# Kernel optimization log

Hardware: AMD Instinct MI355X
Metric: run time of the kernel (lower is better)

The kernel has to match this reference:

```python
import jax, jax.numpy as jnp
import numpy as np


def setup_inputs() -> dict:
    key = jax.random.key(0)
    ks = jax.random.split(key, 7)
    C = 256
    Cqk = C // 8  # 32
    B, D, H, W = 4, 16, 16, 16
    s_in = 1.0 / np.sqrt(C)  # conv1x1 fan_in = C
    return {
        "x": jax.random.normal(ks[0], (B, C, D, H, W), dtype=jnp.float32),
        "Wq": jax.random.uniform(ks[1], (Cqk, C), jnp.float32, -s_in, s_in),
        "bq": jax.random.uniform(ks[2], (Cqk,), jnp.float32, -s_in, s_in),
        "Wk": jax.random.uniform(ks[3], (Cqk, C), jnp.float32, -s_in, s_in),
        "bk": jax.random.uniform(ks[4], (Cqk,), jnp.float32, -s_in, s_in),
        "Wv": jax.random.uniform(ks[5], (C, C), jnp.float32, -s_in, s_in),
        "bv": jax.random.uniform(ks[6], (C,), jnp.float32, -s_in, s_in),
    }


def reference(x, Wq, bq, Wk, bk, Wv, bv):
    B, C, D, H, W = x.shape
    N = D * H * W
    xf = x.reshape(B, C, N)  # [B, C, N]
    # 1x1x1 convs == per-voxel GEMMs over the channel dim
    q = jnp.einsum('oc,bcn->bon', Wq, xf) + bq[None, :, None]  # [B, Cqk, N]
    k = jnp.einsum('oc,bcn->bon', Wk, xf) + bk[None, :, None]  # [B, Cqk, N]
    v = jnp.einsum('oc,bcn->bon', Wv, xf) + bv[None, :, None]  # [B, C, N]
    # attention[b, n, m] = softmax_m( q[:, n] . k[:, m] )
    scores = jnp.einsum('bcn,bcm->bnm', q, k)  # [B, N, N]
    attn = jax.nn.softmax(scores, axis=-1)
    # out = value @ attention^T  -> out[b, c, n] = sum_m v[b,c,m] * attn[b,n,m]
    out = jnp.einsum('bcm,bnm->bcn', v, attn)
    return x + out.reshape(B, C, D, H, W)
```

## Files before the change

kernel.cpp:

```cpp
#include <hip/hip_runtime.h>
#include <math.h>

#define B_   4
#define C_   256
#define CQK  32
#define N_   4096
#define TQ   64
#define TM   64
#define ITERS (N_ / TM)
#define PSS  72

typedef __attribute__((ext_vector_type(8))) short short8;
typedef __attribute__((ext_vector_type(4))) short short4v;
typedef __attribute__((ext_vector_type(4))) float f32x4;
typedef __attribute__((ext_vector_type(2))) unsigned int uint2v;

#if __has_builtin(__builtin_amdgcn_exp2f)
#define EXP2F(x) __builtin_amdgcn_exp2f(x)
#else
#define EXP2F(x) exp2f(x)
#endif

__device__ __forceinline__ unsigned short f2bf(float f) {
    unsigned u = __builtin_bit_cast(unsigned, f);
    u += 0x7fffu + ((u >> 16) & 1u);
    return (unsigned short)(u >> 16);
}

__device__ __forceinline__ unsigned pack2bf(float a, float b) {
    unsigned ua = __builtin_bit_cast(unsigned, a) + 0x8000u;
    unsigned ub = __builtin_bit_cast(unsigned, b) + 0x8000u;
#if __has_builtin(__builtin_amdgcn_perm)
    return __builtin_amdgcn_perm(ub, ua, 0x07060302u);
#else
    return (ua >> 16) | (ub & 0xffff0000u);
#endif
}

__global__ __launch_bounds__(256) void cvt_w(
    const float* __restrict__ Wq, const float* __restrict__ bq,
    const float* __restrict__ Wk, const float* __restrict__ bk,
    const float* __restrict__ Wv, const float* __restrict__ bv,
    unsigned short* __restrict__ wbf, float* __restrict__ biasf)
{
    const float LOG2E = 1.4426950408889634f;
    const int r = blockIdx.x;
    const int t = threadIdx.x;
    const float* src = (r < 32) ? (Wq + r * C_)
                     : (r < 64) ? (Wk + (r - 32) * C_)
                                : (Wv + (r - 64) * C_);
    const float scale = (r < 32) ? LOG2E : 1.0f;
    wbf[r * C_ + t] = f2bf(src[t] * scale);
    if (t == 0)
        biasf[r] = (r < 32) ? bq[r] * LOG2E : (r < 64) ? bk[r - 32] : bv[r - 64];
}

__global__ __launch_bounds__(256, 2) void proj_qkv(
    const float* __restrict__ x, const unsigned short* __restrict__ wbf,
    const float* __restrict__ biasf,
    unsigned short* __restrict__ qb, unsigned short* __restrict__ kb,
    unsigned short* __restrict__ vb)
{
    __shared__ __align__(16) unsigned short qks[32 * 72];

    const int t    = threadIdx.x;
    const int w    = t >> 6;
    const int lane = t & 63;
    const int quad = lane >> 4;
    const int c16  = lane & 15;
    const int n0   = blockIdx.x * 32;
    const int b    = blockIdx.y;

    f32x4 acc[5][2];
#pragma unroll
    for (int i = 0; i < 5; ++i)
#pragma unroll
        for (int nt = 0; nt < 2; ++nt) acc[i][nt] = (f32x4){0.f, 0.f, 0.f, 0.f};

    const float* xb = x + (size_t)(b * C_) * N_ + n0 + c16;
    const unsigned short* wr = wbf + (size_t)(80 * w + c16) * C_ + quad * 8;

#pragma unroll
    for (int h = 0; h < 2; ++h) {
        short8 af[5][4];
#pragma unroll
        for (int i = 0; i < 5; ++i)
#pragma unroll
            for (int k4 = 0; k4 < 4; ++k4)
                af[i][k4] = *(const short8*)(wr + (size_t)(16 * i) * C_ + 128 * h + 32 * k4);
#pragma unroll
        for (int k4 = 0; k4 < 4; ++k4) {
            short8 bf[2];
#pragma unroll
            for (int nt = 0; nt < 2; ++nt) {
                const float* xc = xb + (size_t)(128 * h + 32 * k4 + 8 * quad) * N_ + 16 * nt;
#pragma unroll
                for (int j = 0; j < 8; ++j)
                    bf[nt][j] = (short)f2bf(xc[(size_t)j * N_]);
            }
#pragma unroll
            for (int i = 0; i < 5; ++i)
#pragma unroll
                for (int nt = 0; nt < 2; ++nt)
                    acc[i][nt] = __builtin_amdgcn_mfma_f32_16x16x32_bf16(af[i][k4], bf[nt], acc[i][nt], 0, 0, 0);
        }
    }

#pragma unroll
    for (int i = 0; i < 5; ++i) {
        const int OT = 5 * w + i;
        const int obase = OT * 16 + 4 * quad;
        const f32x4 bv4 = *(const f32x4*)&biasf[obase];
#pragma unroll
        for (int nt = 0; nt < 2; ++nt) {
            const int n = n0 + 16 * nt + c16;
            float vals[4];
#pragma unroll
            for (int r = 0; r < 4; ++r) vals[r] = acc[i][nt][r] + bv4[r];
            if (OT >= 4) {
#pragma unroll
                for (int r = 0; r < 4; ++r)
                    vb[((size_t)(b * C_) + obase + r - 64) * N_ + n] = f2bf(vals[r]);
            } else {
                const int row = 16 * nt + c16;
                const int col = (OT < 2 ? 0 : 32) + (OT & 1) * 16 + 4 * quad;
                short4v pk;
#pragma unroll
                for (int r = 0; r < 4; ++r) pk[r] = (short)f2bf(vals[r]);
                *(short4v*)&qks[row * 72 + col] = pk;
            }
        }
    }
    __syncthreads();
    if (w < 2) {
        unsigned short* dst = w ? kb : qb;
        const int coff = w ? 32 : 0;
#pragma unroll
        for (int h = 0; h < 2; ++h) {
            const int n = 16 * h + (lane >> 2);
            const int c = (lane & 3) * 8;
            const short8 v = *(const short8*)&qks[n * 72 + coff + c];
            *(short8*)(dst + ((size_t)(b * N_) + n0 + n) * 32 + c) = v;
        }
    }
}

__global__ __launch_bounds__(256, 1) void attn_kernel(
    const float* __restrict__ x,
    const unsigned short* __restrict__ qg,
    const unsigned short* __restrict__ kg,
    const unsigned short* __restrict__ vg,
    float* __restrict__ out)
{
    __shared__ __align__(16) unsigned short ps[2][TQ * PSS];
    __shared__ float ls[4 * TQ];

    const int t    = threadIdx.x;
    const int w    = t >> 6;
    const int lane = t & 63;
    const int quad = lane >> 4;
    const int c16  = lane & 15;
    const int b    = blockIdx.x & 3;
    const int q0   = (blockIdx.x >> 2) * TQ;
    const int kvc  = w * 16 + 4 * quad;

    const unsigned short* kbase = kg + (size_t)(b * N_) * 32;
    const unsigned short* vbase = vg + (size_t)(b * C_) * N_;

    short8 bq[4];
#pragma unroll
    for (int g = 0; g < 4; ++g)
        bq[g] = *(const short8*)(qg + ((size_t)(b * N_) + q0 + 16 * g + c16) * 32 + quad * 8);

    f32x4 O[4][4];
#pragma unroll
    for (int ct = 0; ct < 4; ++ct)
#pragma unroll
        for (int qt = 0; qt < 4; ++qt) O[ct][qt] = (f32x4){0.f, 0.f, 0.f, 0.f};

    float lacc[4] = {0.f, 0.f, 0.f, 0.f};

    short8 akA, akB, avA[2][4], avB[2][4];
    akA = *(const short8*)(kbase + (size_t)(w * 16 + c16) * 32 + quad * 8);
#pragma unroll
    for (int s = 0; s < 2; ++s)
#pragma unroll
        for (int ct = 0; ct < 4; ++ct)
            avA[s][ct] = *(const short8*)(
                vbase + (size_t)(64 * w + 16 * ct + c16) * N_ + 32 * s + 8 * quad);

    auto chunk = [&](int ic, const short8& akc, const short8 (&avc)[2][4],
                     short8& akn, short8 (&avn)[2][4], int pb) {
        const int icn = (ic + 1 < ITERS) ? ic + 1 : ITERS - 1;
        const size_t kvn = (size_t)icn * TM;
        akn = *(const short8*)(kbase + (kvn + w * 16 + c16) * 32 + quad * 8);
#pragma unroll
        for (int s = 0; s < 2; ++s)
#pragma unroll
            for (int ct = 0; ct < 4; ++ct)
                avn[s][ct] = *(const short8*)(
                    vbase + (size_t)(64 * w + 16 * ct + c16) * N_ + kvn + 32 * s + 8 * quad);

        const f32x4 z = {0.f, 0.f, 0.f, 0.f};
        f32x4 sf[4];
#pragma unroll
        for (int g = 0; g < 4; ++g)
            sf[g] = __builtin_amdgcn_mfma_f32_16x16x32_bf16(akc, bq[g], z, 0, 0, 0);

#pragma unroll
        for (int g = 0; g < 4; ++g) {
            float p[4];
#pragma unroll
            for (int r = 0; r < 4; ++r) p[r] = EXP2F(sf[g][r]);
            lacc[g] += (p[0] + p[1]) + (p[2] + p[3]);
            uint2v u;
            u.x = pack2bf(p[0], p[1]);
            u.y = pack2bf(p[2], p[3]);
            *(uint2v*)&ps[pb][(16 * g + c16) * PSS + kvc] = u;
        }

        __syncthreads();

        short8 bp[4][2];
#pragma unroll
        for (int qt = 0; qt < 4; ++qt)
#pragma unroll
            for (int s = 0; s < 2; ++s)
                bp[qt][s] = *(const short8*)&ps[pb][(16 * qt + c16) * PSS + 32 * s + 8 * quad];
#pragma unroll
        for (int s = 0; s < 2; ++s)
#pragma unroll
            for (int ct = 0; ct < 4; ++ct)
#pragma unroll
                for (int qt = 0; qt < 4; ++qt)
                    O[ct][qt] = __builtin_amdgcn_mfma_f32_16x16x32_bf16(avc[s][ct], bp[qt][s], O[ct][qt], 0, 0, 0);
    };

#pragma unroll 1
    for (int ic = 0; ic < ITERS; ic += 2) {
        chunk(ic,     akA, avA, akB, avB, 0);
        chunk(ic + 1, akB, avB, akA, avA, 1);
    }

#pragma unroll
    for (int g = 0; g < 4; ++g) {
        lacc[g] += __shfl_xor(lacc[g], 16);
        lacc[g] += __shfl_xor(lacc[g], 32);
    }
    if (quad == 0) {
#pragma unroll
        for (int g = 0; g < 4; ++g)
            ls[w * TQ + 16 * g + c16] = lacc[g];
    }
    __syncthreads();

#pragma unroll
    for (int qt = 0; qt < 4; ++qt) {
        const int q = 16 * qt + c16;
        const float li = 1.0f / (ls[q] + ls[TQ + q] + ls[2 * TQ + q] + ls[3 * TQ + q]);
        const int n = q0 + q;
#pragma unroll
        for (int ct = 0; ct < 4; ++ct) {
#pragma unroll
            for (int r = 0; r < 4; ++r) {
                const int c = 64 * w + 16 * ct + 4 * quad + r;
                const size_t idx = ((size_t)(b * C_) + c) * N_ + n;
                out[idx] = x[idx] + O[ct][qt][r] * li;
            }
        }
    }
}

extern "C" void kernel_launch(void* const* d_in, const int* in_sizes, int n_in,
                              void* d_out, int out_size, void* d_ws, size_t ws_size,
                              hipStream_t stream) {
    const float* x  = (const float*)d_in[0];
    const float* Wq = (const float*)d_in[1];
    const float* bq = (const float*)d_in[2];
    const float* Wk = (const float*)d_in[3];
    const float* bk = (const float*)d_in[4];
    const float* Wv = (const float*)d_in[5];
    const float* bv = (const float*)d_in[6];
    float* out = (float*)d_out;

    unsigned short* ws16 = (unsigned short*)d_ws;
    unsigned short* qb  = ws16;
    unsigned short* kb  = qb + (size_t)B_ * N_ * 32;
    unsigned short* vb  = kb + (size_t)B_ * N_ * 32;
    unsigned short* wbf = vb + (size_t)B_ * C_ * N_;
    float* biasf = (float*)(wbf + 320 * C_);

    cvt_w<<<dim3(320), 256, 0, stream>>>(Wq, bq, Wk, bk, Wv, bv, wbf, biasf);
    proj_qkv<<<dim3(N_ / 32, B_), 256, 0, stream>>>(x, wbf, biasf, qb, kb, vb);
    attn_kernel<<<dim3(N_ / TQ * B_), 256, 0, stream>>>(x, qb, kb, vb, out);
}
```

Baseline: 162.0 us.

## Split attention KV range across blocks, stage K/V in LDS, add combine pass

The attention kernel now runs 512-thread blocks over 128 queries with the key range split in two halves across separate blocks. K and V tiles are staged cooperatively in swizzled shared memory with register prefetch instead of per-wave global loads. A new combine kernel merges the two partial outputs and row sums and adds the residual. The projection kernel transposes and converts x into shared memory once and doubles its tile width. The split-KV scheme costs an extra partial-output write and read (one half in bf16) plus another launch, in exchange for better K/V reuse across waves and a different grid shape.

```diff
diff --git a/kernel.cpp b/kernel.cpp
--- a/kernel.cpp
+++ b/kernel.cpp
@@ -5,10 +5,11 @@
 #define C_   256
 #define CQK  32
 #define N_   4096
-#define TQ   64
+#define TQ   128
 #define TM   64
-#define ITERS (N_ / TM)
+#define HITERS ((N_ / 2) / TM)
 #define PSS  72
+#define XTS  264
 
 typedef __attribute__((ext_vector_type(8))) short short8;
 typedef __attribute__((ext_vector_type(4))) short short4v;
@@ -26,7 +27,9 @@
     u += 0x7fffu + ((u >> 16) & 1u);
     return (unsigned short)(u >> 16);
 }
-
+__device__ __forceinline__ float bf2f(unsigned short s) {
+    return __builtin_bit_cast(float, (unsigned)s << 16);
+}
 __device__ __forceinline__ unsigned pack2bf(float a, float b) {
     unsigned ua = __builtin_bit_cast(unsigned, a) + 0x8000u;
     unsigned ub = __builtin_bit_cast(unsigned, b) + 0x8000u;
@@ -61,49 +64,50 @@
     unsigned short* __restrict__ qb, unsigned short* __restrict__ kb,
     unsigned short* __restrict__ vb)
 {
-    __shared__ __align__(16) unsigned short qks[32 * 72];
+    __shared__ __align__(16) unsigned short xT[64 * XTS];
+    __shared__ __align__(16) unsigned short qks[64 * 72];
 
     const int t    = threadIdx.x;
     const int w    = t >> 6;
     const int lane = t & 63;
     const int quad = lane >> 4;
     const int c16  = lane & 15;
-    const int n0   = blockIdx.x * 32;
+    const int n0   = blockIdx.x * 64;
     const int b    = blockIdx.y;
 
-    f32x4 acc[5][2];
+#pragma unroll
+    for (int p = 0; p < 16; ++p) {
+        const int c  = (t >> 2) + 64 * (p >> 2);
+        const int nq = (t & 3) + 4 * (p & 3);
+        const f32x4 xv = *(const f32x4*)&x[((size_t)(b * C_) + c) * N_ + n0 + 4 * nq];
+#pragma unroll
+        for (int j = 0; j < 4; ++j)
+            xT[(4 * nq + j) * XTS + c] = f2bf(xv[j]);
+    }
+    __syncthreads();
+
+    f32x4 acc[5][4];
 #pragma unroll
     for (int i = 0; i < 5; ++i)
 #pragma unroll
-        for (int nt = 0; nt < 2; ++nt) acc[i][nt] = (f32x4){0.f, 0.f, 0.f, 0.f};
-
-    const float* xb = x + (size_t)(b * C_) * N_ + n0 + c16;
+        for (int nt = 0; nt < 4; ++nt) acc[i][nt] = (f32x4){0.f, 0.f, 0.f, 0.f};
+
     const unsigned short* wr = wbf + (size_t)(80 * w + c16) * C_ + quad * 8;
 
 #pragma unroll
-    for (int h = 0; h < 2; ++h) {
-        short8 af[5][4];
+    for (int ks = 0; ks < 8; ++ks) {
+        short8 af[5], bf[4];
 #pragma unroll
         for (int i = 0; i < 5; ++i)
-#pragma unroll
-            for (int k4 = 0; k4 < 4; ++k4)
-                af[i][k4] = *(const short8*)(wr + (size_t)(16 * i) * C_ + 128 * h + 32 * k4);
-#pragma unroll
-        for (int k4 = 0; k4 < 4; ++k4) {
-            short8 bf[2];
-#pragma unroll
-            for (int nt = 0; nt < 2; ++nt) {
-                const float* xc = xb + (size_t)(128 * h + 32 * k4 + 8 * quad) * N_ + 16 * nt;
-#pragma unroll
-                for (int j = 0; j < 8; ++j)
-                    bf[nt][j] = (short)f2bf(xc[(size_t)j * N_]);
-            }
-#pragma unroll
-            for (int i = 0; i < 5; ++i)
-#pragma unroll
-                for (int nt = 0; nt < 2; ++nt)
-                    acc[i][nt] = __builtin_amdgcn_mfma_f32_16x16x32_bf16(af[i][k4], bf[nt], acc[i][nt], 0, 0, 0);
-        }
+            af[i] = *(const short8*)(wr + (size_t)(16 * i) * C_ + 32 * ks);
+#pragma unroll
+        for (int nt = 0; nt < 4; ++nt)
+            bf[nt] = *(const short8*)&xT[(16 * nt + c16) * XTS + ks * 32 + quad * 8];
+#pragma unroll
+        for (int i = 0; i < 5; ++i)
+#pragma unroll
+            for (int nt = 0; nt < 4; ++nt)
+                acc[i][nt] = __builtin_amdgcn_mfma_f32_16x16x32_bf16(af[i], bf[nt], acc[i][nt], 0, 0, 0);
     }
 
 #pragma unroll
@@ -112,7 +116,7 @@
         const int obase = OT * 16 + 4 * quad;
         const f32x4 bv4 = *(const f32x4*)&biasf[obase];
 #pragma unroll
-        for (int nt = 0; nt < 2; ++nt) {
+        for (int nt = 0; nt < 4; ++nt) {
             const int n = n0 + 16 * nt + c16;
             float vals[4];
 #pragma unroll
@@ -136,7 +140,7 @@
         unsigned short* dst = w ? kb : qb;
         const int coff = w ? 32 : 0;
 #pragma unroll
-        for (int h = 0; h < 2; ++h) {
+        for (int h = 0; h < 4; ++h) {
             const int n = 16 * h + (lane >> 2);
             const int c = (lane & 3) * 8;
             const short8 v = *(const short8*)&qks[n * 72 + coff + c];
@@ -145,14 +149,17 @@
     }
 }
 
-__global__ __launch_bounds__(256, 1) void attn_kernel(
-    const float* __restrict__ x,
+__global__ __launch_bounds__(512, 1) void attn_kernel(
     const unsigned short* __restrict__ qg,
     const unsigned short* __restrict__ kg,
     const unsigned short* __restrict__ vg,
-    float* __restrict__ out)
+    float* __restrict__ outp,
+    unsigned short* __restrict__ Op1,
+    float* __restrict__ lp)
 {
-    __shared__ __align__(16) unsigned short ps[2][TQ * PSS];
+    __shared__ __align__(16) unsigned short ks[TM * 40];
+    __shared__ __align__(16) unsigned short vs[C_ * TM];
+    __shared__ __align__(16) unsigned short ps[TQ * PSS];
     __shared__ float ls[4 * TQ];
 
     const int t    = threadIdx.x;
@@ -160,9 +167,15 @@
     const int lane = t & 63;
     const int quad = lane >> 4;
     const int c16  = lane & 15;
-    const int b    = blockIdx.x & 3;
-    const int q0   = (blockIdx.x >> 2) * TQ;
-    const int kvc  = w * 16 + 4 * quad;
+    const int flat = blockIdx.x;
+    const int half = flat & 1;
+    const int b    = (flat >> 1) & 3;
+    const int q0   = (flat >> 3) * TQ;
+    const int kvb0 = half * (N_ / 2);
+    const int f   = w & 3;
+    const int qg_ = w >> 2;
+    const int cs = w & 3;
+    const int pg = w >> 2;
 
     const unsigned short* kbase = kg + (size_t)(b * N_) * 32;
     const unsigned short* vbase = vg + (size_t)(b * C_) * N_;
@@ -170,7 +183,17 @@
     short8 bq[4];
 #pragma unroll
     for (int g = 0; g < 4; ++g)
-        bq[g] = *(const short8*)(qg + ((size_t)(b * N_) + q0 + 16 * g + c16) * 32 + quad * 8);
+        bq[g] = *(const short8*)(qg + ((size_t)(b * N_) + q0 + 16 * (4 * qg_ + g) + c16) * 32 + quad * 8);
+
+    const int vc0 = t >> 3, vj = t & 7;
+    const int kn = t >> 2, kseg = t & 3;
+
+    short8 vpre[4], kpre;
+#pragma unroll
+    for (int p = 0; p < 4; ++p)
+        vpre[p] = *(const short8*)(vbase + (size_t)(vc0 + 64 * p) * N_ + kvb0 + vj * 8);
+    if (t < 256)
+        kpre = *(const short8*)(kbase + (size_t)(kvb0 + kn) * 32 + kseg * 8);
 
     f32x4 O[4][4];
 #pragma unroll
@@ -180,32 +203,23 @@
 
     float lacc[4] = {0.f, 0.f, 0.f, 0.f};
 
-    short8 akA, akB, avA[2][4], avB[2][4];
-    akA = *(const short8*)(kbase + (size_t)(w * 16 + c16) * 32 + quad * 8);
-#pragma unroll
-    for (int s = 0; s < 2; ++s)
-#pragma unroll
-        for (int ct = 0; ct < 4; ++ct)
-            avA[s][ct] = *(const short8*)(
-                vbase + (size_t)(64 * w + 16 * ct + c16) * N_ + 32 * s + 8 * quad);
-
-    auto chunk = [&](int ic, const short8& akc, const short8 (&avc)[2][4],
-                     short8& akn, short8 (&avn)[2][4], int pb) {
-        const int icn = (ic + 1 < ITERS) ? ic + 1 : ITERS - 1;
-        const size_t kvn = (size_t)icn * TM;
-        akn = *(const short8*)(kbase + (kvn + w * 16 + c16) * 32 + quad * 8);
-#pragma unroll
-        for (int s = 0; s < 2; ++s)
-#pragma unroll
-            for (int ct = 0; ct < 4; ++ct)
-                avn[s][ct] = *(const short8*)(
-                    vbase + (size_t)(64 * w + 16 * ct + c16) * N_ + kvn + 32 * s + 8 * quad);
-
+#pragma unroll 1
+    for (int it = 0; it < HITERS; ++it) {
+#pragma unroll
+        for (int p = 0; p < 4; ++p) {
+            const int c = vc0 + 64 * p;
+            *(short8*)&vs[c * TM + 8 * (vj ^ (c & 7))] = vpre[p];
+        }
+        if (t < 256)
+            *(short8*)&ks[kn * 40 + kseg * 8] = kpre;
+        __syncthreads();
+
+        const short8 ak = *(const short8*)&ks[(16 * f + c16) * 40 + quad * 8];
         const f32x4 z = {0.f, 0.f, 0.f, 0.f};
         f32x4 sf[4];
 #pragma unroll
         for (int g = 0; g < 4; ++g)
-            sf[g] = __builtin_amdgcn_mfma_f32_16x16x32_bf16(akc, bq[g], z, 0, 0, 0);
+            sf[g] = __builtin_amdgcn_mfma_f32_16x16x32_bf16(ak, bq[g], z, 0, 0, 0);
 
 #pragma unroll
         for (int g = 0; g < 4; ++g) {
@@ -216,30 +230,36 @@
             uint2v u;
             u.x = pack2bf(p[0], p[1]);
             u.y = pack2bf(p[2], p[3]);
-            *(uint2v*)&ps[pb][(16 * g + c16) * PSS + kvc] = u;
-        }
-
+            *(uint2v*)&ps[(16 * (4 * qg_ + g) + c16) * PSS + f * 16 + 4 * quad] = u;
+        }
         __syncthreads();
 
+        if (it < HITERS - 1) {
+            const int kv0n = kvb0 + (it + 1) * TM;
+#pragma unroll
+            for (int p = 0; p < 4; ++p)
+                vpre[p] = *(const short8*)(vbase + (size_t)(vc0 + 64 * p) * N_ + kv0n + vj * 8);
+            if (t < 256)
+                kpre = *(const short8*)(kbase + (size_t)(kv0n + kn) * 32 + kseg * 8);
+        }
+
         short8 bp[4][2];
 #pragma unroll
         for (int qt = 0; qt < 4; ++qt)
 #pragma unroll
             for (int s = 0; s < 2; ++s)
-                bp[qt][s] = *(const short8*)&ps[pb][(16 * qt + c16) * PSS + 32 * s + 8 * quad];
+                bp[qt][s] = *(const short8*)&ps[(64 * pg + 16 * qt + c16) * PSS + 32 * s + 8 * quad];
 #pragma unroll
         for (int s = 0; s < 2; ++s)
 #pragma unroll
-            for (int ct = 0; ct < 4; ++ct)
+            for (int ct = 0; ct < 4; ++ct) {
+                const int c = 64 * cs + 16 * ct + c16;
+                const short8 av = *(const short8*)&vs[c * TM + 8 * ((4 * s + quad) ^ (c & 7))];
 #pragma unroll
                 for (int qt = 0; qt < 4; ++qt)
-                    O[ct][qt] = __builtin_amdgcn_mfma_f32_16x16x32_bf16(avc[s][ct], bp[qt][s], O[ct][qt], 0, 0, 0);
-    };
-
-#pragma unroll 1
-    for (int ic = 0; ic < ITERS; ic += 2) {
-        chunk(ic,     akA, avA, akB, avB, 0);
-        chunk(ic + 1, akB, avB, akA, avA, 1);
+                    O[ct][qt] = __builtin_amdgcn_mfma_f32_16x16x32_bf16(av, bp[qt][s], O[ct][qt], 0, 0, 0);
+            }
+        __syncthreads();
     }
 
 #pragma unroll
@@ -250,24 +270,78 @@
     if (quad == 0) {
 #pragma unroll
         for (int g = 0; g < 4; ++g)
-            ls[w * TQ + 16 * g + c16] = lacc[g];
+            ls[f * TQ + 16 * (4 * qg_ + g) + c16] = lacc[g];
     }
     __syncthreads();
 
-#pragma unroll
-    for (int qt = 0; qt < 4; ++qt) {
-        const int q = 16 * qt + c16;
-        const float li = 1.0f / (ls[q] + ls[TQ + q] + ls[2 * TQ + q] + ls[3 * TQ + q]);
-        const int n = q0 + q;
-#pragma unroll
-        for (int ct = 0; ct < 4; ++ct) {
-#pragma unroll
-            for (int r = 0; r < 4; ++r) {
-                const int c = 64 * w + 16 * ct + 4 * quad + r;
-                const size_t idx = ((size_t)(b * C_) + c) * N_ + n;
-                out[idx] = x[idx] + O[ct][qt][r] * li;
+    if (half == 0) {
+        float* ob = outp + (size_t)(b * C_) * N_;
+#pragma unroll
+        for (int ct = 0; ct < 4; ++ct)
+#pragma unroll
+            for (int qt = 0; qt < 4; ++qt) {
+                const int n = q0 + 64 * pg + 16 * qt + c16;
+#pragma unroll
+                for (int r = 0; r < 4; ++r) {
+                    const int c = 64 * cs + 16 * ct + 4 * quad + r;
+                    ob[(size_t)c * N_ + n] = O[ct][qt][r];
+                }
             }
-        }
+    } else {
+        unsigned short* ob = Op1 + (size_t)(b * C_) * N_;
+#pragma unroll
+        for (int ct = 0; ct < 4; ++ct)
+#pragma unroll
+            for (int qt = 0; qt < 4; ++qt) {
+                const int n = q0 + 64 * pg + 16 * qt + c16;
+#pragma unroll
+                for (int r = 0; r < 4; ++r) {
+                    const int c = 64 * cs + 16 * ct + 4 * quad + r;
+                    ob[(size_t)c * N_ + n] = f2bf(O[ct][qt][r]);
+                }
+            }
+    }
+    if (cs == 0) {
+        const int qq = 64 * pg + lane;
+        const float lv = ls[qq] + ls[TQ + qq] + ls[2 * TQ + qq] + ls[3 * TQ + qq];
+        lp[(size_t)(half * B_ + b) * N_ + q0 + qq] = lv;
+    }
+}
+
+__global__ __launch_bounds__(256) void combine_kernel(
+    const float* __restrict__ x,
+    const unsigned short* __restrict__ Op1,
+    const float* __restrict__ lp,
+    float* __restrict__ out)
+{
+    __shared__ float linv[1024];
+
+    const int t  = threadIdx.x;
+    const int n0 = blockIdx.x * 1024;
+    const int c0 = blockIdx.y * 8;
+    const int b  = blockIdx.z;
+
+#pragma unroll
+    for (int i = 0; i < 4; ++i) {
+        const int n = n0 + t + 256 * i;
+        const float l = lp[(size_t)b * N_ + n] + lp[(size_t)(B_ + b) * N_ + n];
+        linv[t + 256 * i] = 1.0f / l;
+    }
+    __syncthreads();
+
+#pragma unroll
+    for (int cc = 0; cc < 8; ++cc) {
+        const int c = c0 + cc;
+        const size_t base = ((size_t)(b * C_) + c) * N_ + n0 + 4 * t;
+        const f32x4 o0 = *(const f32x4*)&out[base];
+        const short4v a1 = *(const short4v*)&Op1[base];
+        const f32x4 xv = *(const f32x4*)&x[base];
+        f32x4 o;
+        o.x = xv.x + (o0.x + bf2f((unsigned short)a1[0])) * linv[4 * t + 0];
+        o.y = xv.y + (o0.y + bf2f((unsigned short)a1[1])) * linv[4 * t + 1];
+        o.z = xv.z + (o0.z + bf2f((unsigned short)a1[2])) * linv[4 * t + 2];
+        o.w = xv.w + (o0.w + bf2f((unsigned short)a1[3])) * linv[4 * t + 3];
+        *(f32x4*)&out[base] = o;
     }
 }
 
@@ -287,10 +361,13 @@
     unsigned short* qb  = ws16;
     unsigned short* kb  = qb + (size_t)B_ * N_ * 32;
     unsigned short* vb  = kb + (size_t)B_ * N_ * 32;
-    unsigned short* wbf = vb + (size_t)B_ * C_ * N_;
+    unsigned short* Op1 = vb + (size_t)B_ * C_ * N_;
+    unsigned short* wbf = Op1 + (size_t)B_ * C_ * N_;
     float* biasf = (float*)(wbf + 320 * C_);
+    float* lpp   = biasf + 320;
 
     cvt_w<<<dim3(320), 256, 0, stream>>>(Wq, bq, Wk, bk, Wv, bv, wbf, biasf);
-    proj_qkv<<<dim3(N_ / 32, B_), 256, 0, stream>>>(x, wbf, biasf, qb, kb, vb);
-    attn_kernel<<<dim3(N_ / TQ * B_), 256, 0, stream>>>(x, qb, kb, vb, out);
-}
+    proj_qkv<<<dim3(N_ / 64, B_), 256, 0, stream>>>(x, wbf, biasf, qb, kb, vb);
+    attn_kernel<<<dim3(256), 512, 0, stream>>>(qb, kb, vb, out, Op1, lpp);
+    combine_kernel<<<dim3(4, 32, B_), 256, 0, stream>>>(x, Op1, lpp, out);
+}
```

Result: faster. 155.0 us (-4.3%).
